# Optimization experiments

Hardware: AMD Instinct MI355X
Metric: run time of the kernel (lower is better)

## Reference

```python
import jax, jax.numpy as jnp
import numpy as np

RHO, MU, DT = 1.0, 0.1, 4.0
AX_X, AX_Y = -1, -2  # x = last axis, y = second-to-last


def first_derivative(f, ax, scheme):
    # unit grid spacing; boundary wrap is irrelevant since [1:-1,1:-1] is sliced off
    if scheme == 'left':
        return f - jnp.roll(f, 1, ax)
    if scheme == 'right':
        return jnp.roll(f, -1, ax) - f
    return 0.5 * (jnp.roll(f, -1, ax) - jnp.roll(f, 1, ax))  # central


def vel_map(f, ax, side):
    # staggered-grid interpolation of velocity to neighboring face
    if side == 'left':
        return 0.5 * (f + jnp.roll(f, 1, ax))
    return 0.5 * (f + jnp.roll(f, -1, ax))


def laplacian(f):
    return (jnp.roll(f, 1, AX_X) + jnp.roll(f, -1, AX_X)
            + jnp.roll(f, 1, AX_Y) + jnp.roll(f, -1, AX_Y) - 4.0 * f)


def setup_inputs() -> dict:
    key = jax.random.key(0)
    k1, k2, k3, k4 = jax.random.split(key, 4)
    B, H, W = 8, 1024, 1024
    return {
        'v_old': jax.random.normal(k1, (B, 2, H, W), dtype=jnp.float32),
        'v_new': jax.random.normal(k2, (B, 2, H, W), dtype=jnp.float32),
        'p_new': jax.random.normal(k3, (B, 1, H, W), dtype=jnp.float32),
        'flow_mask_mac': jax.random.randint(k4, (B, 1, H, W), 0, 2).astype(jnp.int32),
    }


def reference(v_old, v_new, p_new, flow_mask_mac):
    mask = flow_mask_mac.astype(v_old.dtype)
    v = 0.5 * (v_new + v_old)  # integration == 'imex'

    u_old, w_old = v_old[:, 0:1], v_old[:, 1:2]
    u_new, w_new = v_new[:, 0:1], v_new[:, 1:2]
    u, w = v[:, 0:1], v[:, 1:2]

    # x-momentum residual (channel 1)
    res_x = mask * (RHO * ((w_new - w_old) / DT
                           + w * first_derivative(w, AX_X, 'central')
                           + 0.5 * (vel_map(u, AX_X, 'left') * first_derivative(w, AX_Y, 'left')
                                    + vel_map(u, AX_X, 'right') * first_derivative(w, AX_Y, 'right')))
                    + first_derivative(p_new, AX_X, 'left')
                    - MU * laplacian(w))

    # y-momentum residual (channel 0)
    res_y = mask * (RHO * ((u_new - u_old) / DT
                           + u * first_derivative(u, AX_Y, 'central')
                           + 0.5 * (vel_map(w, AX_Y, 'left') * first_derivative(u, AX_X, 'left')
                                    + vel_map(w, AX_Y, 'right') * first_derivative(u, AX_X, 'right')))
                    + first_derivative(p_new, AX_Y, 'left')
                    - MU * laplacian(u))

    loss_x = jnp.mean(jnp.square(res_x)[:, :, 1:-1, 1:-1], axis=(1, 2, 3))
    loss_y = jnp.mean(jnp.square(res_y)[:, :, 1:-1, 1:-1], axis=(1, 2, 3))
    return loss_x + loss_y  # shape [B]
```

## Files before the change

kernel.cpp:

```cpp
#include <hip/hip_runtime.h>


#define NS_H 1024
#define NS_W 1024
#define INT_ROWS (NS_H - 2)

__device__ __forceinline__ float4 ld4(const float* p) { return *(const float4*)p; }

__global__ __launch_bounds__(256) void ns_loss_partial(
    const float* __restrict__ v_old,
    const float* __restrict__ v_new,
    const float* __restrict__ p,
    const int*   __restrict__ mask,
    float* __restrict__ ws)
{
    const int blk = blockIdx.x;
    const int b = blk / INT_ROWS;
    const int y = 1 + (blk % INT_ROWS);

    const size_t hw = (size_t)NS_H * NS_W;
    const float* uo = v_old + (size_t)b * 2 * hw;
    const float* wo = uo + hw;
    const float* un = v_new + (size_t)b * 2 * hw;
    const float* wn = un + hw;
    const float* pb = p    + (size_t)b * hw;
    const int*   mb = mask + (size_t)b * hw;

    const int x0 = (int)threadIdx.x * 4;
    const int rm = (y - 1) * NS_W, rc = y * NS_W, rp = (y + 1) * NS_W;

    float4 unc = ld4(un + rc + x0), uoc = ld4(uo + rc + x0);
    float  unl = un[rc + x0 - 1],   uol = uo[rc + x0 - 1];
    float  unr = un[rc + x0 + 4],   uor = uo[rc + x0 + 4];
    float4 wnc = ld4(wn + rc + x0), woc = ld4(wo + rc + x0);
    float  wnl = wn[rc + x0 - 1],   wol = wo[rc + x0 - 1];
    float  wnr = wn[rc + x0 + 4],   wor = wo[rc + x0 + 4];
    float4 unm = ld4(un + rm + x0), uom = ld4(uo + rm + x0);
    float4 unp = ld4(un + rp + x0), uop = ld4(uo + rp + x0);
    float4 wnm = ld4(wn + rm + x0), wom = ld4(wo + rm + x0);
    float4 wnp = ld4(wn + rp + x0), wop = ld4(wo + rp + x0);
    float4 pc4 = ld4(pb + rc + x0);
    float  p_l = pb[rc + x0 - 1];
    float4 pym4 = ld4(pb + rm + x0);
    int4   m4  = *(const int4*)(mb + rc + x0);

    const float uc[6] = {0.5f*(unl+uol), 0.5f*(unc.x+uoc.x), 0.5f*(unc.y+uoc.y),
                         0.5f*(unc.z+uoc.z), 0.5f*(unc.w+uoc.w), 0.5f*(unr+uor)};
    const float wc[6] = {0.5f*(wnl+wol), 0.5f*(wnc.x+woc.x), 0.5f*(wnc.y+woc.y),
                         0.5f*(wnc.z+woc.z), 0.5f*(wnc.w+woc.w), 0.5f*(wnr+wor)};
    const float uym[4] = {0.5f*(unm.x+uom.x), 0.5f*(unm.y+uom.y), 0.5f*(unm.z+uom.z), 0.5f*(unm.w+uom.w)};
    const float uyp[4] = {0.5f*(unp.x+uop.x), 0.5f*(unp.y+uop.y), 0.5f*(unp.z+uop.z), 0.5f*(unp.w+uop.w)};
    const float wym[4] = {0.5f*(wnm.x+wom.x), 0.5f*(wnm.y+wom.y), 0.5f*(wnm.z+wom.z), 0.5f*(wnm.w+wom.w)};
    const float wyp[4] = {0.5f*(wnp.x+wop.x), 0.5f*(wnp.y+wop.y), 0.5f*(wnp.z+wop.z), 0.5f*(wnp.w+wop.w)};
    const float du[4]  = {unc.x-uoc.x, unc.y-uoc.y, unc.z-uoc.z, unc.w-uoc.w};
    const float dw[4]  = {wnc.x-woc.x, wnc.y-woc.y, wnc.z-woc.z, wnc.w-woc.w};
    const float pc[5]  = {p_l, pc4.x, pc4.y, pc4.z, pc4.w};
    const float pym[4] = {pym4.x, pym4.y, pym4.z, pym4.w};
    const int   mm[4]  = {m4.x, m4.y, m4.z, m4.w};

    float acc = 0.f;
    #pragma unroll
    for (int j = 0; j < 4; ++j) {
        const int x = x0 + j;
        const float m = (x >= 1 && x <= NS_W - 2) ? (float)mm[j] : 0.f;

        const float u_c = uc[j+1], u_xm = uc[j], u_xp = uc[j+2];
        const float w_c = wc[j+1], w_xm = wc[j], w_xp = wc[j+2];

        float res_x =
            dw[j] * 0.25f
          + w_c * 0.5f * (w_xp - w_xm)
          + 0.5f * ( 0.5f * (u_c + u_xm) * (w_c    - wym[j])
                   + 0.5f * (u_c + u_xp) * (wyp[j] - w_c   ) )
          + (pc[j+1] - pc[j])
          - 0.1f * (w_xm + w_xp + wym[j] + wyp[j] - 4.f * w_c);

        float res_y =
            du[j] * 0.25f
          + u_c * 0.5f * (uyp[j] - uym[j])
          + 0.5f * ( 0.5f * (w_c + wym[j]) * (u_c  - u_xm)
                   + 0.5f * (w_c + wyp[j]) * (u_xp - u_c ) )
          + (pc[j+1] - pym[j])
          - 0.1f * (u_xm + u_xp + uym[j] + uyp[j] - 4.f * u_c);

        acc += m * (res_x * res_x + res_y * res_y);
    }

    #pragma unroll
    for (int off = 32; off > 0; off >>= 1)
        acc += __shfl_down(acc, off);

    __shared__ float smem[4];
    const int lane = threadIdx.x & 63;
    const int wid  = threadIdx.x >> 6;
    if (lane == 0) smem[wid] = acc;
    __syncthreads();

    if (threadIdx.x == 0)
        ws[blk] = smem[0] + smem[1] + smem[2] + smem[3];
}

__global__ __launch_bounds__(256) void ns_loss_reduce(
    const float* __restrict__ ws, float* __restrict__ out)
{
    const int b = blockIdx.x;
    float acc = 0.f;
    for (int i = threadIdx.x; i < INT_ROWS; i += 256)
        acc += ws[b * INT_ROWS + i];

    #pragma unroll
    for (int off = 32; off > 0; off >>= 1)
        acc += __shfl_down(acc, off);

    __shared__ float smem[4];
    const int lane = threadIdx.x & 63;
    const int wid  = threadIdx.x >> 6;
    if (lane == 0) smem[wid] = acc;
    __syncthreads();

    if (threadIdx.x == 0) {
        const float inv = 1.0f / ((float)INT_ROWS * (float)(NS_W - 2));
        out[b] = (smem[0] + smem[1] + smem[2] + smem[3]) * inv;
    }
}

extern "C" void kernel_launch(void* const* d_in, const int* in_sizes, int n_in,
                              void* d_out, int out_size, void* d_ws, size_t ws_size,
                              hipStream_t stream) {
    const float* v_old = (const float*)d_in[0];
    const float* v_new = (const float*)d_in[1];
    const float* p_new = (const float*)d_in[2];
    const int*   msk   = (const int*)d_in[3];
    float* out = (float*)d_out;
    float* ws  = (float*)d_ws;

    const int B = out_size;

    ns_loss_partial<<<dim3(B * INT_ROWS), dim3(256), 0, stream>>>(v_old, v_new, p_new, msk, ws);
    ns_loss_reduce<<<dim3(B), dim3(256), 0, stream>>>(ws, out);
}
```

Baseline: 206.4 us.

## Process row strips per block with rolling register window and shuffle halos

Each block now handles a strip of 7 interior rows instead of one. It keeps the previous, current and next row averages in registers and slides them down, so each row is loaded about once instead of three times. Left and right halo values come from wavefront shuffles, with scalar loads only at wave edges. This cuts redundant global and L2 traffic and the count of tiny blocks, and adds launch bounds for occupancy. The cost is fewer, longer blocks and more register pressure. The correctness of 1022 = 146*7 relies on the exact grid size.

```diff
diff --git a/kernel.cpp b/kernel.cpp
--- a/kernel.cpp
+++ b/kernel.cpp
@@ -3,11 +3,18 @@
 
 #define NS_H 1024
 #define NS_W 1024
-#define INT_ROWS (NS_H - 2)
+#define ROWS 7
+#define STRIPS ((NS_H - 2) / ROWS)
 
 __device__ __forceinline__ float4 ld4(const float* p) { return *(const float4*)p; }
+__device__ __forceinline__ float4 avg4(float4 a, float4 b) {
+    return make_float4(0.5f*(a.x+b.x), 0.5f*(a.y+b.y), 0.5f*(a.z+b.z), 0.5f*(a.w+b.w));
+}
+__device__ __forceinline__ float4 sub4(float4 a, float4 b) {
+    return make_float4(a.x-b.x, a.y-b.y, a.z-b.z, a.w-b.w);
+}
 
-__global__ __launch_bounds__(256) void ns_loss_partial(
+__global__ __launch_bounds__(256, 4) void ns_loss_partial(
     const float* __restrict__ v_old,
     const float* __restrict__ v_new,
     const float* __restrict__ p,
@@ -15,8 +22,9 @@
     float* __restrict__ ws)
 {
     const int blk = blockIdx.x;
-    const int b = blk / INT_ROWS;
-    const int y = 1 + (blk % INT_ROWS);
+    const int b  = blk / STRIPS;
+    const int rb = blk % STRIPS;
+    const int y0 = 1 + rb * ROWS;
 
     const size_t hw = (size_t)NS_H * NS_W;
     const float* uo = v_old + (size_t)b * 2 * hw;
@@ -26,64 +34,110 @@
     const float* pb = p    + (size_t)b * hw;
     const int*   mb = mask + (size_t)b * hw;
 
-    const int x0 = (int)threadIdx.x * 4;
-    const int rm = (y - 1) * NS_W, rc = y * NS_W, rp = (y + 1) * NS_W;
+    const int tid  = (int)threadIdx.x;
+    const int x0   = tid * 4;
+    const int lane = tid & 63;
 
-    float4 unc = ld4(un + rc + x0), uoc = ld4(uo + rc + x0);
-    float  unl = un[rc + x0 - 1],   uol = uo[rc + x0 - 1];
-    float  unr = un[rc + x0 + 4],   uor = uo[rc + x0 + 4];
-    float4 wnc = ld4(wn + rc + x0), woc = ld4(wo + rc + x0);
-    float  wnl = wn[rc + x0 - 1],   wol = wo[rc + x0 - 1];
-    float  wnr = wn[rc + x0 + 4],   wor = wo[rc + x0 + 4];
-    float4 unm = ld4(un + rm + x0), uom = ld4(uo + rm + x0);
-    float4 unp = ld4(un + rp + x0), uop = ld4(uo + rp + x0);
-    float4 wnm = ld4(wn + rm + x0), wom = ld4(wo + rm + x0);
-    float4 wnp = ld4(wn + rp + x0), wop = ld4(wo + rp + x0);
-    float4 pc4 = ld4(pb + rc + x0);
-    float  p_l = pb[rc + x0 - 1];
-    float4 pym4 = ld4(pb + rm + x0);
-    int4   m4  = *(const int4*)(mb + rc + x0);
+    const int r_m = (y0 - 1) * NS_W;
+    const int r_c = y0 * NS_W;
 
-    const float uc[6] = {0.5f*(unl+uol), 0.5f*(unc.x+uoc.x), 0.5f*(unc.y+uoc.y),
-                         0.5f*(unc.z+uoc.z), 0.5f*(unc.w+uoc.w), 0.5f*(unr+uor)};
-    const float wc[6] = {0.5f*(wnl+wol), 0.5f*(wnc.x+woc.x), 0.5f*(wnc.y+woc.y),
-                         0.5f*(wnc.z+woc.z), 0.5f*(wnc.w+woc.w), 0.5f*(wnr+wor)};
-    const float uym[4] = {0.5f*(unm.x+uom.x), 0.5f*(unm.y+uom.y), 0.5f*(unm.z+uom.z), 0.5f*(unm.w+uom.w)};
-    const float uyp[4] = {0.5f*(unp.x+uop.x), 0.5f*(unp.y+uop.y), 0.5f*(unp.z+uop.z), 0.5f*(unp.w+uop.w)};
-    const float wym[4] = {0.5f*(wnm.x+wom.x), 0.5f*(wnm.y+wom.y), 0.5f*(wnm.z+wom.z), 0.5f*(wnm.w+wom.w)};
-    const float wyp[4] = {0.5f*(wnp.x+wop.x), 0.5f*(wnp.y+wop.y), 0.5f*(wnp.z+wop.z), 0.5f*(wnp.w+wop.w)};
-    const float du[4]  = {unc.x-uoc.x, unc.y-uoc.y, unc.z-uoc.z, unc.w-uoc.w};
-    const float dw[4]  = {wnc.x-woc.x, wnc.y-woc.y, wnc.z-woc.z, wnc.w-woc.w};
-    const float pc[5]  = {p_l, pc4.x, pc4.y, pc4.z, pc4.w};
-    const float pym[4] = {pym4.x, pym4.y, pym4.z, pym4.w};
-    const int   mm[4]  = {m4.x, m4.y, m4.z, m4.w};
+    float4 a, bb, c, d;
+    a = ld4(un + r_m + x0); bb = ld4(uo + r_m + x0);
+    c = ld4(wn + r_m + x0); d  = ld4(wo + r_m + x0);
+    float4 u_m = avg4(a, bb), w_m = avg4(c, d);
+
+    a = ld4(un + r_c + x0); bb = ld4(uo + r_c + x0);
+    c = ld4(wn + r_c + x0); d  = ld4(wo + r_c + x0);
+    float4 u_c = avg4(a, bb), w_c = avg4(c, d);
+    float4 du_c = sub4(a, bb), dw_c = sub4(c, d);
+
+    float ul_c = __shfl_up(u_c.w, 1);
+    float wl_c = __shfl_up(w_c.w, 1);
+    if (lane == 0 && x0 > 0) {
+        ul_c = 0.5f * (un[r_c + x0 - 1] + uo[r_c + x0 - 1]);
+        wl_c = 0.5f * (wn[r_c + x0 - 1] + wo[r_c + x0 - 1]);
+    }
+    float ur_c = __shfl_down(u_c.x, 1);
+    float wr_c = __shfl_down(w_c.x, 1);
+    if (lane == 63 && x0 < NS_W - 4) {
+        ur_c = 0.5f * (un[r_c + x0 + 4] + uo[r_c + x0 + 4]);
+        wr_c = 0.5f * (wn[r_c + x0 + 4] + wo[r_c + x0 + 4]);
+    }
+    float4 p_m = ld4(pb + r_m + x0);
 
     float acc = 0.f;
+
     #pragma unroll
-    for (int j = 0; j < 4; ++j) {
-        const int x = x0 + j;
-        const float m = (x >= 1 && x <= NS_W - 2) ? (float)mm[j] : 0.f;
+    for (int r = 0; r < ROWS; ++r) {
+        const int rc = (y0 + r) * NS_W;
+        const int rp = rc + NS_W;
 
-        const float u_c = uc[j+1], u_xm = uc[j], u_xp = uc[j+2];
-        const float w_c = wc[j+1], w_xm = wc[j], w_xp = wc[j+2];
+        a = ld4(un + rp + x0); bb = ld4(uo + rp + x0);
+        c = ld4(wn + rp + x0); d  = ld4(wo + rp + x0);
+        float4 pc4 = ld4(pb + rc + x0);
+        int4   m4  = *(const int4*)(mb + rc + x0);
 
-        float res_x =
-            dw[j] * 0.25f
-          + w_c * 0.5f * (w_xp - w_xm)
-          + 0.5f * ( 0.5f * (u_c + u_xm) * (w_c    - wym[j])
-                   + 0.5f * (u_c + u_xp) * (wyp[j] - w_c   ) )
-          + (pc[j+1] - pc[j])
-          - 0.1f * (w_xm + w_xp + wym[j] + wyp[j] - 4.f * w_c);
+        float4 u_p = avg4(a, bb), w_p = avg4(c, d);
+        float4 du_p = sub4(a, bb), dw_p = sub4(c, d);
 
-        float res_y =
-            du[j] * 0.25f
-          + u_c * 0.5f * (uyp[j] - uym[j])
-          + 0.5f * ( 0.5f * (w_c + wym[j]) * (u_c  - u_xm)
-                   + 0.5f * (w_c + wyp[j]) * (u_xp - u_c ) )
-          + (pc[j+1] - pym[j])
-          - 0.1f * (u_xm + u_xp + uym[j] + uyp[j] - 4.f * u_c);
+        float ul_p = __shfl_up(u_p.w, 1);
+        float wl_p = __shfl_up(w_p.w, 1);
+        if (lane == 0 && x0 > 0) {
+            ul_p = 0.5f * (un[rp + x0 - 1] + uo[rp + x0 - 1]);
+            wl_p = 0.5f * (wn[rp + x0 - 1] + wo[rp + x0 - 1]);
+        }
+        float ur_p = __shfl_down(u_p.x, 1);
+        float wr_p = __shfl_down(w_p.x, 1);
+        if (lane == 63 && x0 < NS_W - 4) {
+            ur_p = 0.5f * (un[rp + x0 + 4] + uo[rp + x0 + 4]);
+            wr_p = 0.5f * (wn[rp + x0 + 4] + wo[rp + x0 + 4]);
+        }
+        float pl = __shfl_up(pc4.w, 1);
+        if (lane == 0 && x0 > 0) pl = pb[rc + x0 - 1];
 
-        acc += m * (res_x * res_x + res_y * res_y);
+        const float uc[6]  = {ul_c, u_c.x, u_c.y, u_c.z, u_c.w, ur_c};
+        const float wcv[6] = {wl_c, w_c.x, w_c.y, w_c.z, w_c.w, wr_c};
+        const float uym[4] = {u_m.x, u_m.y, u_m.z, u_m.w};
+        const float uyp[4] = {u_p.x, u_p.y, u_p.z, u_p.w};
+        const float wym[4] = {w_m.x, w_m.y, w_m.z, w_m.w};
+        const float wyp[4] = {w_p.x, w_p.y, w_p.z, w_p.w};
+        const float du[4]  = {du_c.x, du_c.y, du_c.z, du_c.w};
+        const float dw[4]  = {dw_c.x, dw_c.y, dw_c.z, dw_c.w};
+        const float pcv[5] = {pl, pc4.x, pc4.y, pc4.z, pc4.w};
+        const float pym[4] = {p_m.x, p_m.y, p_m.z, p_m.w};
+        const int   mm[4]  = {m4.x, m4.y, m4.z, m4.w};
+
+        #pragma unroll
+        for (int j = 0; j < 4; ++j) {
+            const int x = x0 + j;
+            const float m = (x >= 1 && x <= NS_W - 2) ? (float)mm[j] : 0.f;
+
+            const float u_cc = uc[j+1],  u_xm = uc[j],  u_xp = uc[j+2];
+            const float w_cc = wcv[j+1], w_xm = wcv[j], w_xp = wcv[j+2];
+
+            float res_x =
+                dw[j] * 0.25f
+              + w_cc * 0.5f * (w_xp - w_xm)
+              + 0.5f * ( 0.5f * (u_cc + u_xm) * (w_cc   - wym[j])
+                       + 0.5f * (u_cc + u_xp) * (wyp[j] - w_cc  ) )
+              + (pcv[j+1] - pcv[j])
+              - 0.1f * (w_xm + w_xp + wym[j] + wyp[j] - 4.f * w_cc);
+
+            float res_y =
+                du[j] * 0.25f
+              + u_cc * 0.5f * (uyp[j] - uym[j])
+              + 0.5f * ( 0.5f * (w_cc + wym[j]) * (u_cc - u_xm)
+                       + 0.5f * (w_cc + wyp[j]) * (u_xp - u_cc) )
+              + (pcv[j+1] - pym[j])
+              - 0.1f * (u_xm + u_xp + uym[j] + uyp[j] - 4.f * u_cc);
+
+            acc += m * (res_x * res_x + res_y * res_y);
+        }
+
+        u_m = u_c;  u_c = u_p;  ul_c = ul_p;  ur_c = ur_p;
+        w_m = w_c;  w_c = w_p;  wl_c = wl_p;  wr_c = wr_p;
+        du_c = du_p; dw_c = dw_p;
+        p_m = pc4;
     }
 
     #pragma unroll
@@ -91,12 +145,11 @@
         acc += __shfl_down(acc, off);
 
     __shared__ float smem[4];
-    const int lane = threadIdx.x & 63;
-    const int wid  = threadIdx.x >> 6;
+    const int wid = tid >> 6;
     if (lane == 0) smem[wid] = acc;
     __syncthreads();
 
-    if (threadIdx.x == 0)
+    if (tid == 0)
         ws[blk] = smem[0] + smem[1] + smem[2] + smem[3];
 }
 
@@ -105,8 +158,8 @@
 {
     const int b = blockIdx.x;
     float acc = 0.f;
-    for (int i = threadIdx.x; i < INT_ROWS; i += 256)
-        acc += ws[b * INT_ROWS + i];
+    for (int i = threadIdx.x; i < STRIPS; i += 256)
+        acc += ws[b * STRIPS + i];
 
     #pragma unroll
     for (int off = 32; off > 0; off >>= 1)
@@ -119,7 +172,7 @@
     __syncthreads();
 
     if (threadIdx.x == 0) {
-        const float inv = 1.0f / ((float)INT_ROWS * (float)(NS_W - 2));
+        const float inv = 1.0f / ((float)(NS_H - 2) * (float)(NS_W - 2));
         out[b] = (smem[0] + smem[1] + smem[2] + smem[3]) * inv;
     }
 }
@@ -136,6 +189,6 @@
 
     const int B = out_size;
 
-    ns_loss_partial<<<dim3(B * INT_ROWS), dim3(256), 0, stream>>>(v_old, v_new, p_new, msk, ws);
+    ns_loss_partial<<<dim3(B * STRIPS), dim3(256), 0, stream>>>(v_old, v_new, p_new, msk, ws);
     ns_loss_reduce<<<dim3(B), dim3(256), 0, stream>>>(ws, out);
 }
```

Measured after the change: 327.0 us. +58.4%, slower.
